# Kernel optimization log

Hardware: AMD Instinct MI355X
Metric: run time of the kernel (lower is better)

The kernel has to match this reference:

```python
import jax, jax.numpy as jnp
import numpy as np

SIZE = 48   # grid side
D = 2       # neighborhood radius
LOOP = 1    # number of full sweeps
K = 2 * D + 1  # kernel side (5)
BATCH = 8192


def setup_inputs() -> dict:
    key = jax.random.key(0)
    k1, k2 = jax.random.split(key)
    inputs = jax.random.normal(k1, (BATCH, SIZE * SIZE), dtype=jnp.float32)
    # nn.Parameter init: uniform in [-0.5, 0.5]
    weights = jax.random.uniform(k2, (SIZE, SIZE, K, K), dtype=jnp.float32,
                                 minval=-0.5, maxval=0.5)
    return {"inputs": inputs, "weights": weights}


def _cell_order():
    # Matches torch loop order: loop outer, x middle, y inner.
    coords = np.array([(y, x)
                       for _ in range(LOOP)
                       for x in range(D, SIZE - D)
                       for y in range(D, SIZE - D)], dtype=np.int32)
    return jnp.asarray(coords[:, 0]), jnp.asarray(coords[:, 1])


def _run(grid, weights):
    # grid: (B, SIZE, SIZE); sequential per-cell scatter-add via lax.scan.
    ys, xs = _cell_order()
    wseq = weights[ys, xs]  # (steps, K, K), differentiable gather
    B = grid.shape[0]

    def step(g, inp):
        y0, x0, w = inp  # y0 = y - D, x0 = x - D (top-left of patch)
        patch = jax.lax.dynamic_slice(g, (0, y0, x0), (B, K, K))
        v = patch[:, D, D]                     # center value, read first
        patch = patch.at[:, D, D].set(0.0)     # zero center
        patch = patch + v[:, None, None] * w   # scatter-add v * weights[y, x]
        g = jax.lax.dynamic_update_slice(g, patch, (0, y0, x0))
        return g, None

    grid, _ = jax.lax.scan(step, grid, (ys - D, xs - D, wseq))
    return grid


def reference(inputs, weights):
    B = inputs.shape[0]
    grid = inputs.reshape(B, SIZE, SIZE)
    grid = _run(grid, weights)
    return grid.reshape(B, -1)
```

## Files before the change

### kernel.cpp

```cpp
#include <hip/hip_runtime.h>


#define SZ 48
#define DP 2
#define NC (SZ * SZ)
#define NBATCH 4
#define GS 2308
#define PADH 104
#define NSTEP 173
#define TSTEPS 180
#define NT 64

#define NINT 1936
#define NINT_ALLOC 2048
#define NBOR 368
#define NBOR_ALLOC 448

#define WF_FLOATS (TSTEPS * 16 * 12)
#define FI_FLOATS (NINT_ALLOC * 16)
#define FB_FLOATS (NBOR_ALLOC * 24)

__device__ __forceinline__ bool is_in(int v) {
    return (unsigned)(v - DP) <= (unsigned)(SZ - 2 * DP - 1);
}

__global__ void prep_kernel(const float* __restrict__ w, float* __restrict__ ws)
{
    int id = blockIdx.x * 256 + threadIdx.x;
    float* WFseq = ws;
    float* FIc   = ws + WF_FLOATS;
    float* FBc   = FIc + FI_FLOATS;

    if (id < TSTEPS * 16) {
        int t = id >> 4, s = id & 15;
        float vals[12];
        #pragma unroll
        for (int k = 0; k < 12; ++k) vals[k] = 0.f;
        if (t < NSTEP) {
            int xlo = (t > 43) ? (t - 41) / 3 : 0;
            int xhi = t / 3; if (xhi > 43) xhi = 43;
            int x2 = xlo + s;
            if (x2 <= xhi) {
                int y2 = t - 3 * x2;
                int y = y2 + DP, x = x2 + DP, c = y * SZ + x;
                const int edy[12] = {-2,-1, 0, 1, 2, -2,-1, 0, 1, 2, -2,-1};
                const int edx[12] = {-2,-2,-2,-2,-2, -1,-1,-1,-1,-1,  0, 0};
                #pragma unroll
                for (int k = 0; k < 12; ++k) {
                    int dy = edy[k], dx = edx[k];
                    if (is_in(y + dy) && is_in(x + dx)) {
                        int nc = c + dy * SZ + dx;
                        vals[k] = w[nc * 25 + (DP - dy) * 5 + (DP - dx)];
                    }
                }
            }
        }
        float* o = WFseq + id * 12;
        #pragma unroll
        for (int k = 0; k < 12; ++k) o[k] = vals[k];
        return;
    }
    int id2 = id - TSTEPS * 16;
    if (id2 < NINT_ALLOC) {
        float vals[16];
        #pragma unroll
        for (int k = 0; k < 16; ++k) vals[k] = 0.f;
        if (id2 < NINT) {
            int y2 = id2 / 44, x2 = id2 - y2 * 44;
            int y = y2 + DP, x = x2 + DP, c = y * SZ + x;
            vals[0] = w[c * 25 + 12];
            const int ldy[12] = { 1, 2, -2,-1, 0, 1, 2, -2,-1, 0, 1, 2};
            const int ldx[12] = { 0, 0,  1, 1, 1, 1, 1,  2, 2, 2, 2, 2};
            #pragma unroll
            for (int k = 0; k < 12; ++k) {
                int dy = ldy[k], dx = ldx[k];
                if (is_in(y + dy) && is_in(x + dx)) {
                    int nc = c + dy * SZ + dx;
                    vals[1 + k] = w[nc * 25 + (DP - dy) * 5 + (DP - dx)];
                }
            }
        }
        float* o = FIc + id2 * 16;
        #pragma unroll
        for (int k = 0; k < 16; ++k) o[k] = vals[k];
        return;
    }
    int id3 = id2 - NINT_ALLOC;
    if (id3 < NBOR_ALLOC) {
        float vals[24];
        #pragma unroll
        for (int k = 0; k < 24; ++k) vals[k] = 0.f;
        if (id3 < NBOR) {
            int y, x;
            if (id3 < 96)       { y = id3 / 48;             x = id3 - (id3 / 48) * 48; }
            else if (id3 < 192) { int j = id3 - 96;  y = 46 + j / 48; x = j - (j / 48) * 48; }
            else                { int j = id3 - 192; y = 2 + (j >> 2); int q = j & 3; x = q + (q >= 2 ? 44 : 0); }
            int c = y * SZ + x;
            int k = 0;
            #pragma unroll
            for (int dy = -2; dy <= 2; ++dy) {
                #pragma unroll
                for (int dx = -2; dx <= 2; ++dx) {
                    if (dy == 0 && dx == 0) continue;
                    if (is_in(y + dy) && is_in(x + dx)) {
                        int nc = c + dy * SZ + dx;
                        vals[k] = w[nc * 25 + (DP - dy) * 5 + (DP - dx)];
                    }
                    ++k;
                }
            }
        }
        float* o = FBc + id3 * 24;
        #pragma unroll
        for (int k = 0; k < 24; ++k) o[k] = vals[k];
    }
}

__device__ __forceinline__ void do_step(int tt, int s, float* gb,
                                        float4 w0, float4 w1, float4 w2)
{
    int xlo = (tt > 43) ? (tt - 41) / 3 : 0;
    int xhi = tt / 3; if (xhi > 43) xhi = 43;
    int x2 = xlo + s;
    if (x2 <= xhi) {
        int cell = (tt - 3 * x2 + DP) * SZ + x2 + DP;
        const float* p = gb + cell - 98;
        float a0 = w0.x * p[0]   + w0.y * p[48]  + w0.z * p[96] + w0.w * p[144];
        float a1 = w1.x * p[192] + w1.y * p[1]   + w1.z * p[49] + w1.w * p[97];
        float a2 = w2.x * p[145] + w2.y * p[193] + w2.z * p[2]  + w2.w * p[50];
        gb[cell] = p[98] + a0 + a1 + a2;
    }
}

__device__ __forceinline__ void loadw(const float* wfbase, int tt,
                                      float4& w0, float4& w1, float4& w2)
{
    const float4* q = (const float4*)(wfbase + tt * 192);
    w0 = q[0]; w1 = q[1]; w2 = q[2];
}

__global__ __launch_bounds__(NT)
void ca_kernel(const float* __restrict__ in, const float* __restrict__ ws,
               float* __restrict__ out)
{
    __shared__ float gmem[PADH + NBATCH * GS + PADH];
    float* g = gmem + PADH;
    const int tid = threadIdx.x;
    const int b0  = blockIdx.x * NBATCH;

    for (int i = tid; i < PADH; i += NT) { gmem[i] = 0.f; gmem[PADH + NBATCH * GS + i] = 0.f; }
    #pragma unroll
    for (int b = 0; b < NBATCH; ++b) {
        const float4* src = (const float4*)(in + (size_t)(b0 + b) * NC);
        float4* dst = (float4*)(g + b * GS);
        for (int i = tid; i < NC / 4; i += NT) dst[i] = src[i];
    }

    const int bl = tid & (NBATCH - 1);
    const int s  = tid >> 2;
    float* gb = g + bl * GS;
    const float* wfbase = ws + s * 12;

    float4 A0, A1, A2, B0, B1, B2, C0, C1, C2, D0, D1, D2;
    loadw(wfbase, 0, A0, A1, A2);
    loadw(wfbase, 1, B0, B1, B2);
    loadw(wfbase, 2, C0, C1, C2);
    loadw(wfbase, 3, D0, D1, D2);
    for (int t = 0; t < 176; t += 4) {
        do_step(t + 0, s, gb, A0, A1, A2);  loadw(wfbase, t + 4, A0, A1, A2);
        do_step(t + 1, s, gb, B0, B1, B2);  loadw(wfbase, t + 5, B0, B1, B2);
        do_step(t + 2, s, gb, C0, C1, C2);  loadw(wfbase, t + 6, C0, C1, C2);
        do_step(t + 3, s, gb, D0, D1, D2);  loadw(wfbase, t + 7, D0, D1, D2);
    }

    const float* FIc = ws + WF_FLOATS;
    const float* FBc = FIc + FI_FLOATS;

    {
        const float4* fp = (const float4*)(FIc + tid * 16);
        float4 f0 = fp[0], f1 = fp[1], f2 = fp[2], f3 = fp[3];
        for (int it = 0; it < 31; ++it) {
            int idx = it * NT + tid;
            const float4* np = (const float4*)(FIc + (idx + NT) * 16);
            float4 n0 = np[0], n1 = np[1], n2 = np[2], n3 = np[3];
            if (idx < NINT) {
                int y2 = idx / 44, x2 = idx - y2 * 44;
                int c = (y2 + DP) * SZ + x2 + DP;
                #pragma unroll
                for (int b = 0; b < NBATCH; ++b) {
                    const float* p = g + b * GS + c - 95;
                    float o = f0.x * p[95]  + f0.y * p[143] + f0.z * p[191] + f0.w * p[0]
                            + f1.x * p[48]  + f1.y * p[96]  + f1.z * p[144] + f1.w * p[192]
                            + f2.x * p[1]   + f2.y * p[49]  + f2.z * p[97]  + f2.w * p[145]
                            + f3.x * p[193];
                    out[(size_t)(b0 + b) * NC + c] = o;
                }
            }
            f0 = n0; f1 = n1; f2 = n2; f3 = n3;
        }
    }

    {
        const float4* fp = (const float4*)(FBc + tid * 24);
        float4 f0 = fp[0], f1 = fp[1], f2 = fp[2], f3 = fp[3], f4 = fp[4], f5 = fp[5];
        for (int it = 0; it < 6; ++it) {
            int idx = it * NT + tid;
            const float4* np = (const float4*)(FBc + (idx + NT) * 24);
            float4 n0 = np[0], n1 = np[1], n2 = np[2], n3 = np[3], n4 = np[4], n5 = np[5];
            if (idx < NBOR) {
                int y, x;
                if (idx < 96)       { y = idx / 48;            x = idx - (idx / 48) * 48; }
                else if (idx < 192) { int j = idx - 96;  y = 46 + j / 48; x = j - (j / 48) * 48; }
                else                { int j = idx - 192; y = 2 + (j >> 2); int q = j & 3; x = q + (q >= 2 ? 44 : 0); }
                int c = y * SZ + x;
                #pragma unroll
                for (int b = 0; b < NBATCH; ++b) {
                    const float* p = g + b * GS + c - 98;
                    float o = p[98]
                        + f0.x * p[0]   + f0.y * p[1]   + f0.z * p[2]   + f0.w * p[3]
                        + f1.x * p[4]   + f1.y * p[48]  + f1.z * p[49]  + f1.w * p[50]
                        + f2.x * p[51]  + f2.y * p[52]  + f2.z * p[96]  + f2.w * p[97]
                        + f3.x * p[99]  + f3.y * p[100] + f3.z * p[144] + f3.w * p[145]
                        + f4.x * p[146] + f4.y * p[147] + f4.z * p[148] + f4.w * p[192]
                        + f5.x * p[193] + f5.y * p[194] + f5.z * p[195] + f5.w * p[196];
                    out[(size_t)(b0 + b) * NC + c] = o;
                }
            }
            f0 = n0; f1 = n1; f2 = n2; f3 = n3; f4 = n4; f5 = n5;
        }
    }
}

extern "C" void kernel_launch(void* const* d_in, const int* in_sizes, int n_in,
                              void* d_out, int out_size, void* d_ws, size_t ws_size,
                              hipStream_t stream)
{
    const float* in = (const float*)d_in[0];
    const float* w  = (const float*)d_in[1];
    float* out = (float*)d_out;
    float* ws  = (float*)d_ws;

    const int batch   = in_sizes[0] / NC;
    const int nblocks = batch / NBATCH;

    prep_kernel<<<21, 256, 0, stream>>>(w, ws);
    ca_kernel<<<nblocks, NT, 0, stream>>>(in, ws, out);
}
```

Baseline: 276.0 us.

## Overlap interior finalize with sequential sweep using producer/consumer wavefronts

Doubles the block to two wavefronts: wave 0 runs the sequential anti-diagonal sweep while wave 1 computes the interior output cells a fixed number of diagonal steps behind, synchronised with a per-phase barrier. Finalize weights are reordered into sweep-step order so the consumer can follow the wavefront. The aim is to hide the separate finalize pass behind the latency-bound sequential sweep. The cost is per-phase barriers, a larger block that may lower occupancy, and reliance on a lag of 12 steps being enough for correctness.

```diff
diff --git a/kernel.cpp b/kernel.cpp
--- a/kernel.cpp
+++ b/kernel.cpp
@@ -7,17 +7,16 @@
 #define NBATCH 4
 #define GS 2308
 #define PADH 104
-#define NSTEP 173
+#define NT 128
+#define NPHASE 47
+
 #define TSTEPS 180
-#define NT 64
-
-#define NINT 1936
-#define NINT_ALLOC 2048
+#define FTSTEPS 184
 #define NBOR 368
-#define NBOR_ALLOC 448
+#define NBOR_ALLOC 512
 
 #define WF_FLOATS (TSTEPS * 16 * 12)
-#define FI_FLOATS (NINT_ALLOC * 16)
+#define FW_FLOATS (FTSTEPS * 16 * 16)
 #define FB_FLOATS (NBOR_ALLOC * 24)
 
 __device__ __forceinline__ bool is_in(int v) {
@@ -28,15 +27,15 @@
 {
     int id = blockIdx.x * 256 + threadIdx.x;
     float* WFseq = ws;
-    float* FIc   = ws + WF_FLOATS;
-    float* FBc   = FIc + FI_FLOATS;
+    float* FWseq = ws + WF_FLOATS;
+    float* FBc   = FWseq + FW_FLOATS;
 
     if (id < TSTEPS * 16) {
         int t = id >> 4, s = id & 15;
         float vals[12];
         #pragma unroll
         for (int k = 0; k < 12; ++k) vals[k] = 0.f;
-        if (t < NSTEP) {
+        if (t < 173) {
             int xlo = (t > 43) ? (t - 41) / 3 : 0;
             int xhi = t / 3; if (xhi > 43) xhi = 43;
             int x2 = xlo + s;
@@ -61,31 +60,37 @@
         return;
     }
     int id2 = id - TSTEPS * 16;
-    if (id2 < NINT_ALLOC) {
+    if (id2 < FTSTEPS * 16) {
+        int t = id2 >> 4, s = id2 & 15;
         float vals[16];
         #pragma unroll
         for (int k = 0; k < 16; ++k) vals[k] = 0.f;
-        if (id2 < NINT) {
-            int y2 = id2 / 44, x2 = id2 - y2 * 44;
-            int y = y2 + DP, x = x2 + DP, c = y * SZ + x;
-            vals[0] = w[c * 25 + 12];
-            const int ldy[12] = { 1, 2, -2,-1, 0, 1, 2, -2,-1, 0, 1, 2};
-            const int ldx[12] = { 0, 0,  1, 1, 1, 1, 1,  2, 2, 2, 2, 2};
-            #pragma unroll
-            for (int k = 0; k < 12; ++k) {
-                int dy = ldy[k], dx = ldx[k];
-                if (is_in(y + dy) && is_in(x + dx)) {
-                    int nc = c + dy * SZ + dx;
-                    vals[1 + k] = w[nc * 25 + (DP - dy) * 5 + (DP - dx)];
-                }
-            }
-        }
-        float* o = FIc + id2 * 16;
+        if (t < 173) {
+            int xlo = (t > 43) ? (t - 41) / 3 : 0;
+            int xhi = t / 3; if (xhi > 43) xhi = 43;
+            int x2 = xlo + s;
+            if (x2 <= xhi) {
+                int y2 = t - 3 * x2;
+                int y = y2 + DP, x = x2 + DP, c = y * SZ + x;
+                vals[0] = w[c * 25 + 12];
+                const int ldy[12] = { 1, 2, -2,-1, 0, 1, 2, -2,-1, 0, 1, 2};
+                const int ldx[12] = { 0, 0,  1, 1, 1, 1, 1,  2, 2, 2, 2, 2};
+                #pragma unroll
+                for (int k = 0; k < 12; ++k) {
+                    int dy = ldy[k], dx = ldx[k];
+                    if (is_in(y + dy) && is_in(x + dx)) {
+                        int nc = c + dy * SZ + dx;
+                        vals[1 + k] = w[nc * 25 + (DP - dy) * 5 + (DP - dx)];
+                    }
+                }
+            }
+        }
+        float* o = FWseq + id2 * 16;
         #pragma unroll
         for (int k = 0; k < 16; ++k) o[k] = vals[k];
         return;
     }
-    int id3 = id2 - NINT_ALLOC;
+    int id3 = id2 - FTSTEPS * 16;
     if (id3 < NBOR_ALLOC) {
         float vals[24];
         #pragma unroll
@@ -132,11 +137,49 @@
     }
 }
 
-__device__ __forceinline__ void loadw(const float* wfbase, int tt,
-                                      float4& w0, float4& w1, float4& w2)
-{
-    const float4* q = (const float4*)(wfbase + tt * 192);
+__device__ __forceinline__ void loadw3(const float* wfbase, int tt,
+                                       float4& w0, float4& w1, float4& w2)
+{
+    int ci = tt < TSTEPS - 1 ? tt : TSTEPS - 1;
+    const float4* q = (const float4*)(wfbase + ci * 192);
     w0 = q[0]; w1 = q[1]; w2 = q[2];
+}
+
+__device__ __forceinline__ void fin_step(int tt, int s, const float* gb, float* outp,
+                                         float4 f0, float4 f1, float4 f2, float4 f3)
+{
+    if ((unsigned)tt > 172u) return;
+    int xlo = (tt > 43) ? (tt - 41) / 3 : 0;
+    int xhi = tt / 3; if (xhi > 43) xhi = 43;
+    int x2 = xlo + s;
+    if (x2 <= xhi) {
+        int cell = (tt - 3 * x2 + DP) * SZ + x2 + DP;
+        const float* p = gb + cell - 95;
+        float o = f0.x * p[95]  + f0.y * p[143] + f0.z * p[191] + f0.w * p[0]
+                + f1.x * p[48]  + f1.y * p[96]  + f1.z * p[144] + f1.w * p[192]
+                + f2.x * p[1]   + f2.y * p[49]  + f2.z * p[97]  + f2.w * p[145]
+                + f3.x * p[193];
+        outp[cell] = o;
+    }
+}
+
+__device__ __forceinline__ void loadw4(const float* fwbase, int tt,
+                                       float4& f0, float4& f1, float4& f2, float4& f3)
+{
+    int ci = tt < 0 ? 0 : (tt < FTSTEPS - 1 ? tt : FTSTEPS - 1);
+    const float4* q = (const float4*)(fwbase + ci * 256);
+    f0 = q[0]; f1 = q[1]; f2 = q[2]; f3 = q[3];
+}
+
+__device__ __forceinline__ void publish_barrier() {
+    asm volatile("s_waitcnt lgkmcnt(0)" ::: "memory");
+    __builtin_amdgcn_s_barrier();
+    asm volatile("" ::: "memory");
+}
+__device__ __forceinline__ void consume_barrier() {
+    asm volatile("" ::: "memory");
+    __builtin_amdgcn_s_barrier();
+    asm volatile("" ::: "memory");
 }
 
 __global__ __launch_bounds__(NT)
@@ -155,55 +198,52 @@
         float4* dst = (float4*)(g + b * GS);
         for (int i = tid; i < NC / 4; i += NT) dst[i] = src[i];
     }
-
-    const int bl = tid & (NBATCH - 1);
-    const int s  = tid >> 2;
+    __syncthreads();
+
+    const int wid  = tid >> 6;
+    const int lane = tid & 63;
+    const int bl   = lane & (NBATCH - 1);
+    const int s    = lane >> 2;
     float* gb = g + bl * GS;
-    const float* wfbase = ws + s * 12;
-
-    float4 A0, A1, A2, B0, B1, B2, C0, C1, C2, D0, D1, D2;
-    loadw(wfbase, 0, A0, A1, A2);
-    loadw(wfbase, 1, B0, B1, B2);
-    loadw(wfbase, 2, C0, C1, C2);
-    loadw(wfbase, 3, D0, D1, D2);
-    for (int t = 0; t < 176; t += 4) {
-        do_step(t + 0, s, gb, A0, A1, A2);  loadw(wfbase, t + 4, A0, A1, A2);
-        do_step(t + 1, s, gb, B0, B1, B2);  loadw(wfbase, t + 5, B0, B1, B2);
-        do_step(t + 2, s, gb, C0, C1, C2);  loadw(wfbase, t + 6, C0, C1, C2);
-        do_step(t + 3, s, gb, D0, D1, D2);  loadw(wfbase, t + 7, D0, D1, D2);
-    }
-
-    const float* FIc = ws + WF_FLOATS;
-    const float* FBc = FIc + FI_FLOATS;
+
+    if (wid == 0) {
+        const float* wfbase = ws + s * 12;
+        float4 A0, A1, A2, B0, B1, B2, C0, C1, C2, D0, D1, D2;
+        loadw3(wfbase, 0, A0, A1, A2);
+        loadw3(wfbase, 1, B0, B1, B2);
+        loadw3(wfbase, 2, C0, C1, C2);
+        loadw3(wfbase, 3, D0, D1, D2);
+        for (int p = 0; p < NPHASE; ++p) {
+            int t = p * 4;
+            do_step(t + 0, s, gb, A0, A1, A2);  loadw3(wfbase, t + 4, A0, A1, A2);
+            do_step(t + 1, s, gb, B0, B1, B2);  loadw3(wfbase, t + 5, B0, B1, B2);
+            do_step(t + 2, s, gb, C0, C1, C2);  loadw3(wfbase, t + 6, C0, C1, C2);
+            do_step(t + 3, s, gb, D0, D1, D2);  loadw3(wfbase, t + 7, D0, D1, D2);
+            publish_barrier();
+        }
+    } else {
+        const float* fwbase = ws + WF_FLOATS + s * 16;
+        float* outp = out + (size_t)(b0 + bl) * NC;
+        float4 A0, A1, A2, A3, B0, B1, B2, B3, C0, C1, C2, C3, D0, D1, D2, D3;
+        loadw4(fwbase, -12, A0, A1, A2, A3);
+        loadw4(fwbase, -11, B0, B1, B2, B3);
+        loadw4(fwbase, -10, C0, C1, C2, C3);
+        loadw4(fwbase,  -9, D0, D1, D2, D3);
+        for (int p = 0; p < NPHASE; ++p) {
+            int tau = p * 4 - 12;
+            fin_step(tau + 0, s, gb, outp, A0, A1, A2, A3);  loadw4(fwbase, tau + 4, A0, A1, A2, A3);
+            fin_step(tau + 1, s, gb, outp, B0, B1, B2, B3);  loadw4(fwbase, tau + 5, B0, B1, B2, B3);
+            fin_step(tau + 2, s, gb, outp, C0, C1, C2, C3);  loadw4(fwbase, tau + 6, C0, C1, C2, C3);
+            fin_step(tau + 3, s, gb, outp, D0, D1, D2, D3);  loadw4(fwbase, tau + 7, D0, D1, D2, D3);
+            consume_barrier();
+        }
+    }
 
     {
-        const float4* fp = (const float4*)(FIc + tid * 16);
-        float4 f0 = fp[0], f1 = fp[1], f2 = fp[2], f3 = fp[3];
-        for (int it = 0; it < 31; ++it) {
-            int idx = it * NT + tid;
-            const float4* np = (const float4*)(FIc + (idx + NT) * 16);
-            float4 n0 = np[0], n1 = np[1], n2 = np[2], n3 = np[3];
-            if (idx < NINT) {
-                int y2 = idx / 44, x2 = idx - y2 * 44;
-                int c = (y2 + DP) * SZ + x2 + DP;
-                #pragma unroll
-                for (int b = 0; b < NBATCH; ++b) {
-                    const float* p = g + b * GS + c - 95;
-                    float o = f0.x * p[95]  + f0.y * p[143] + f0.z * p[191] + f0.w * p[0]
-                            + f1.x * p[48]  + f1.y * p[96]  + f1.z * p[144] + f1.w * p[192]
-                            + f2.x * p[1]   + f2.y * p[49]  + f2.z * p[97]  + f2.w * p[145]
-                            + f3.x * p[193];
-                    out[(size_t)(b0 + b) * NC + c] = o;
-                }
-            }
-            f0 = n0; f1 = n1; f2 = n2; f3 = n3;
-        }
-    }
-
-    {
+        const float* FBc = ws + WF_FLOATS + FW_FLOATS;
         const float4* fp = (const float4*)(FBc + tid * 24);
         float4 f0 = fp[0], f1 = fp[1], f2 = fp[2], f3 = fp[3], f4 = fp[4], f5 = fp[5];
-        for (int it = 0; it < 6; ++it) {
+        for (int it = 0; it < 3; ++it) {
             int idx = it * NT + tid;
             const float4* np = (const float4*)(FBc + (idx + NT) * 24);
             float4 n0 = np[0], n1 = np[1], n2 = np[2], n3 = np[3], n4 = np[4], n5 = np[5];
@@ -243,6 +283,6 @@
     const int batch   = in_sizes[0] / NC;
     const int nblocks = batch / NBATCH;
 
-    prep_kernel<<<21, 256, 0, stream>>>(w, ws);
+    prep_kernel<<<25, 256, 0, stream>>>(w, ws);
     ca_kernel<<<nblocks, NT, 0, stream>>>(in, ws, out);
 }
```

Measured after the change: 358.6 us. +29.9%, slower.
